# Kernel optimization log

Hardware: AMD Instinct MI355X
Metric: run time of the kernel (lower is better)

The kernel has to match this reference:

```python
import jax, jax.numpy as jnp
import numpy as np

B, L, D, P = 8, 2048, 1024, 4  # batch, length, word_dim, phrase_len


def setup_inputs() -> dict:
    key = jax.random.key(0)
    kx, kw, kb = jax.random.split(key, 3)
    x = jax.random.normal(kx, (B, L, D), dtype=jnp.float32)
    # torch nn.Linear(phrase_dim, word_dim): W [out=D, in=D*P], b [D]
    scale = 1.0 / np.sqrt(D * P)
    W = jax.random.uniform(kw, (D, D * P), dtype=jnp.float32, minval=-scale, maxval=scale)
    b = jax.random.uniform(kb, (D,), dtype=jnp.float32, minval=-scale, maxval=scale)
    return {"x": x, "W": W, "b": b}


def reference(x, W, b):
    Bs, Ls, Ds = x.shape
    Ps = W.shape[1] // Ds  # phrase_len
    # gram[i][:, t] = x[:, t - i] (zero for t < i): left-pad by i, keep first L steps.
    # Stack on the LAST axis then reshape, matching torch's contiguous view over
    # (dim, phrase_len) -> feature index d*P + i.
    grams = jnp.stack(
        [jnp.pad(x, ((0, 0), (i, 0), (0, 0)))[:, :Ls, :] for i in range(Ps)],
        axis=-1,
    )  # [B, L, D, P]
    feat = grams.reshape(Bs, Ls, Ds * Ps)  # [B, L, D*P]
    # nn.Linear: y = feat @ W.T + b
    return jnp.einsum("blf,df->bld", feat, W) + b
```

## Files before the change

### kernel.cpp

```cpp
#include <hip/hip_runtime.h>
#include <hip/hip_bf16.h>
#include <stdint.h>

#define Bq 8
#define Lq 2048
#define Dq 1024
#define Pq 4
#define Kq 4096
#define LPAD 2056
#define BM 256
#define BN 256
#define BK 64

typedef __attribute__((ext_vector_type(8))) short short8;
typedef __attribute__((ext_vector_type(4))) float f32x4;

__device__ __forceinline__ unsigned short f2bf(float f) {
  unsigned u = __float_as_uint(f);
  u += 0x7FFFu + ((u >> 16) & 1u);
  return (unsigned short)(u >> 16);
}

__device__ __forceinline__ void gload_lds16(const void* g, void* l) {
  __builtin_amdgcn_global_load_lds(
      (const __attribute__((address_space(1))) void*)g,
      (__attribute__((address_space(3))) void*)l, 16, 0, 0);
}

__global__ void k_prep(const float* __restrict__ x, const float* __restrict__ W,
                       unsigned short* __restrict__ xp, unsigned short* __restrict__ Wp) {
  if (blockIdx.x < 8224u) {
    unsigned g = blockIdx.x * blockDim.x + threadIdx.x;
    unsigned base = g * 8;
    const unsigned total = (unsigned)Bq * LPAD * Dq;
    if (base >= total) return;
    unsigned t = base >> 10;
    unsigned b = t / LPAD;
    unsigned r = t - b * LPAD;
    unsigned d = base & 1023;
    short8 o;
    if (r >= 3 && r < 3 + Lq) {
      const float* s = x + ((size_t)b * Lq + (r - 3)) * Dq + d;
      float4 v0 = *(const float4*)(s);
      float4 v1 = *(const float4*)(s + 4);
      o[0] = (short)f2bf(v0.x); o[1] = (short)f2bf(v0.y);
      o[2] = (short)f2bf(v0.z); o[3] = (short)f2bf(v0.w);
      o[4] = (short)f2bf(v1.x); o[5] = (short)f2bf(v1.y);
      o[6] = (short)f2bf(v1.z); o[7] = (short)f2bf(v1.w);
    } else {
      o = (short8)0;
    }
    *(short8*)(xp + base) = o;
  } else {
    unsigned g = (blockIdx.x - 8224u) * blockDim.x + threadIdx.x;
    unsigned base = g * 8;
    unsigned d = base >> 12;
    unsigned rem = base & 4095;
    unsigned dp = rem >> 2;
    const float4* src = (const float4*)(W + base);
    float4 v0 = src[0];
    float4 v1 = src[1];
    float a0[4] = {v0.x, v0.y, v0.z, v0.w};
    float a1[4] = {v1.x, v1.y, v1.z, v1.w};
#pragma unroll
    for (int i = 0; i < 4; ++i) {
      unsigned packed = (unsigned)f2bf(a0[i]) | ((unsigned)f2bf(a1[i]) << 16);
      *(unsigned*)(Wp + (size_t)d * 4096 + (size_t)i * 1024 + dp) = packed;
    }
  }
}


#define VM8 asm volatile("s_waitcnt vmcnt(8)" ::: "memory")
#define VM2 asm volatile("s_waitcnt vmcnt(2)" ::: "memory")
#define VM0 asm volatile("s_waitcnt vmcnt(0)" ::: "memory")
#define BAR __builtin_amdgcn_s_barrier()
#define NOPS ((void)0)

#define STAGE_A(buf, kt, h) do { \
    const unsigned scl_ = ((((unsigned)(bRow0 + (h) * 64 - ((kt) >> 4))) << 10) + (((unsigned)(kt) & 15u) << 6)) << 1; \
    _Pragma("unroll") for (int q_ = 0; q_ < 2; ++q_) \
      gload_lds16((const char*)xp + (thrA[q_] + scl_), \
                  lds + ((buf) << 15) + ((h) << 14) + (q_ << 13) + (tid << 4)); \
  } while (0)

#define STAGE_B(buf, kt, h) do { \
    const unsigned scl_ = ((((unsigned)(n0 + (h) * 32)) << 12) + ((unsigned)(kt) << 6)) << 1; \
    _Pragma("unroll") for (int q_ = 0; q_ < 2; ++q_) \
      gload_lds16((const char*)Wp + (thrB[q_] + scl_), \
                  lds + 65536 + ((buf) << 15) + ((h) << 14) + (q_ << 13) + (tid << 4)); \
  } while (0)

#define READ_A(dst, buf, h) do { \
    _Pragma("unroll") for (int mi = 0; mi < 4; ++mi) \
    _Pragma("unroll") for (int kk = 0; kk < 2; ++kk) \
      dst[mi][kk] = *(const short8*)(lds + (((buf) << 15) + ((h) << 14)) + aRC[mi][kk]); \
  } while (0)

#define READ_B(dst, buf, h) do { \
    _Pragma("unroll") for (int ni = 0; ni < 2; ++ni) \
    _Pragma("unroll") for (int kk = 0; kk < 2; ++kk) \
      dst[ni][kk] = *(const short8*)(lds + (((buf) << 15) + ((h) << 14)) + bRC[ni][kk]); \
  } while (0)

#define MFMA_PAIR(mh) do { \
    __builtin_amdgcn_s_setprio(1); \
    _Pragma("unroll") for (int kk = 0; kk < 2; ++kk) { \
      _Pragma("unroll") for (int mi = 0; mi < 4; ++mi) \
      _Pragma("unroll") for (int ni = 0; ni < 2; ++ni) \
        acc[(mh) * 4 + mi][ni] = __builtin_amdgcn_mfma_f32_16x16x32_bf16( \
            fa[mi][kk], bX[ni][kk], acc[(mh) * 4 + mi][ni], 0, 0, 0); \
      _Pragma("unroll") for (int mi = 0; mi < 4; ++mi) \
      _Pragma("unroll") for (int ni = 0; ni < 2; ++ni) \
        acc[(mh) * 4 + mi][2 + ni] = __builtin_amdgcn_mfma_f32_16x16x32_bf16( \
            fa[mi][kk], bY[ni][kk], acc[(mh) * 4 + mi][2 + ni], 0, 0, 0); \
    } \
    __builtin_amdgcn_s_setprio(0); \
  } while (0)

__global__ void __launch_bounds__(512, 2)
k_gemm(const unsigned short* __restrict__ xp,
       const unsigned short* __restrict__ Wp,
       const float* __restrict__ bias,
       float* __restrict__ out) {
  __shared__ __attribute__((aligned(16))) unsigned char lds[131072];

  const int tid  = threadIdx.x;
  const int lane = tid & 63;
  const int w    = tid >> 6;
  const int wm   = w >> 2;
  const int wn   = w & 3;

  const int bid = blockIdx.x;
  const int swz = (bid & 7) * 32 + (bid >> 3);
  const int m0 = (swz >> 2) * BM;
  const int n0 = (swz & 3) * BN;
  const int b  = m0 >> 11;
  const int l0 = m0 & 2047;
  const int bRow0 = b * LPAD + l0 + 3;

  const int sr0 = tid >> 3;
  const unsigned clog = ((unsigned)((tid & 7) ^ (sr0 & 7))) << 3;
  unsigned thrA[2], thrB[2];
  const unsigned nb0 = (((unsigned)sr0 >> 5) << 6) + ((unsigned)sr0 & 31);
#pragma unroll
  for (int q = 0; q < 2; ++q) {
    thrA[q] = ((((unsigned)(sr0 + q * 128)) << 10) + clog) << 1;
    thrB[q] = (((nb0 + q * 128u) << 12) + clog) << 1;
  }

  int aRC[4][2], bRC[2][2];
  {
    int colByte[2];
#pragma unroll
    for (int kk = 0; kk < 2; ++kk)
      colByte[kk] = (kk * 64 + ((lane >> 4) << 4)) ^ ((lane & 7) << 4);
#pragma unroll
    for (int mi = 0; mi < 4; ++mi)
#pragma unroll
      for (int kk = 0; kk < 2; ++kk)
        aRC[mi][kk] = ((wm * 64 + mi * 16 + (lane & 15)) << 7) + colByte[kk];
#pragma unroll
    for (int ni = 0; ni < 2; ++ni)
#pragma unroll
      for (int kk = 0; kk < 2; ++kk)
        bRC[ni][kk] = 65536 + ((wn * 32 + ni * 16 + (lane & 15)) << 7) + colByte[kk];
  }

  f32x4 acc[8][4] = {};
  short8 fa[4][2], bX[2][2], bY[2][2];

  STAGE_A(0, 0, 0);
  STAGE_B(0, 0, 0);
  STAGE_B(0, 0, 1);
  STAGE_A(0, 0, 1);
  STAGE_A(1, 1, 0);
  STAGE_B(1, 1, 0);
  STAGE_B(1, 1, 1);
  VM8;
  BAR;

#pragma unroll 1
  for (int it = 0; it < 31; ++it) {
    const int T = it * 2;
    READ_A(fa, 0, 0); READ_B(bX, 0, 0); READ_B(bY, 0, 1);
    STAGE_A(1, T + 1, 1);
    MFMA_PAIR(0);
    VM8;
    BAR;
    READ_A(fa, 0, 1);
    STAGE_A(0, T + 2, 0); STAGE_B(0, T + 2, 0); STAGE_B(0, T + 2, 1);
    MFMA_PAIR(1);
    VM8;
    BAR;
    READ_A(fa, 1, 0); READ_B(bX, 1, 0); READ_B(bY, 1, 1);
    STAGE_A(0, T + 2, 1);
    MFMA_PAIR(0);
    VM8;
    BAR;
    READ_A(fa, 1, 1);
    STAGE_A(1, T + 3, 0); STAGE_B(1, T + 3, 0); STAGE_B(1, T + 3, 1);
    MFMA_PAIR(1);
    VM8;
    BAR;
  }

  READ_A(fa, 0, 0); READ_B(bX, 0, 0); READ_B(bY, 0, 1);
  STAGE_A(1, 63, 1);
  MFMA_PAIR(0);
  VM8;
  BAR;
  READ_A(fa, 0, 1);
  MFMA_PAIR(1);
  VM2;
  BAR;
  READ_A(fa, 1, 0); READ_B(bX, 1, 0); READ_B(bY, 1, 1);
  MFMA_PAIR(0);
  VM0;
  BAR;
  READ_A(fa, 1, 1);
  MFMA_PAIR(1);

#pragma unroll
  for (int nig = 0; nig < 4; ++nig) {
    const int col = n0 + wn * 64 + nig * 16 + (lane & 15);
    const float bv = bias[col];
#pragma unroll
    for (int mig = 0; mig < 8; ++mig) {
      const int row0 = m0 + wm * 128 + mig * 16 + ((lane >> 4) << 2);
#pragma unroll
      for (int t2 = 0; t2 < 4; ++t2)
        out[(size_t)(row0 + t2) * Dq + col] = acc[mig][nig][t2] + bv;
    }
  }
}

__global__ void k_naive(const float* __restrict__ x, const float* __restrict__ W,
                        const float* __restrict__ bias, float* __restrict__ out) {
  size_t g = (size_t)blockIdx.x * blockDim.x + threadIdx.x;
  const size_t total = (size_t)Bq * Lq * Dq;
  if (g >= total) return;
  int d = (int)(g & 1023);
  int l = (int)((g >> 10) & 2047);
  int b = (int)(g >> 21);
  float s = bias[d];
  for (int i = 0; i < Pq; ++i) {
    if (l - i < 0) continue;
    const float* xr = x + ((size_t)b * Lq + (l - i)) * Dq;
    const float* wr = W + (size_t)d * Kq + i;
    float accv = 0.f;
    for (int dp = 0; dp < Dq; ++dp) accv += xr[dp] * wr[(size_t)dp * 4];
    s += accv;
  }
  out[g] = s;
}

extern "C" void kernel_launch(void* const* d_in, const int* in_sizes, int n_in,
                              void* d_out, int out_size, void* d_ws, size_t ws_size,
                              hipStream_t stream) {
  const float* x    = (const float*)d_in[0];
  const float* W    = (const float*)d_in[1];
  const float* bias = (const float*)d_in[2];
  float* out = (float*)d_out;

  const size_t WP_BYTES = (size_t)Dq * Kq * sizeof(unsigned short);
  const size_t XP_BYTES = (size_t)Bq * LPAD * Dq * sizeof(unsigned short);

  if (ws_size < WP_BYTES + XP_BYTES) {
    const size_t total = (size_t)Bq * Lq * Dq;
    k_naive<<<(unsigned)((total + 255) / 256), 256, 0, stream>>>(x, W, bias, out);
    return;
  }

  unsigned short* Wp = (unsigned short*)d_ws;
  unsigned short* xp = (unsigned short*)((char*)d_ws + WP_BYTES);

  k_prep<<<10272, 256, 0, stream>>>(x, W, xp, Wp);
  k_gemm<<<dim3((Bq * Lq / BM) * (Dq / BN)), 512, 0, stream>>>(xp, Wp, bias, out);
}
```

Before: 129.0 us.

## Double-buffer register fragments to overlap LDS reads with MFMA

Splits the A and B register fragments into two alternating sets, so the LDS reads for the next half-step are issued before the current MFMA batch runs instead of right after a barrier. The vmcnt waits are retuned to match the new staging order. Launch bounds drop to one block per SM so the extra fragment registers fit. The cost is a much larger register footprint and lower occupancy, which reduces latency hiding across blocks.

```diff
diff --git a/kernel.cpp b/kernel.cpp
--- a/kernel.cpp
+++ b/kernel.cpp
@@ -71,11 +71,10 @@
 }
 
 
-#define VM8 asm volatile("s_waitcnt vmcnt(8)" ::: "memory")
+#define VM6 asm volatile("s_waitcnt vmcnt(6)" ::: "memory")
 #define VM2 asm volatile("s_waitcnt vmcnt(2)" ::: "memory")
 #define VM0 asm volatile("s_waitcnt vmcnt(0)" ::: "memory")
 #define BAR __builtin_amdgcn_s_barrier()
-#define NOPS ((void)0)
 
 #define STAGE_A(buf, kt, h) do { \
     const unsigned scl_ = ((((unsigned)(bRow0 + (h) * 64 - ((kt) >> 4))) << 10) + (((unsigned)(kt) & 15u) << 6)) << 1; \
@@ -103,22 +102,22 @@
       dst[ni][kk] = *(const short8*)(lds + (((buf) << 15) + ((h) << 14)) + bRC[ni][kk]); \
   } while (0)
 
-#define MFMA_PAIR(mh) do { \
+#define MFMA_PAIR(mh, A, BX, BY) do { \
     __builtin_amdgcn_s_setprio(1); \
     _Pragma("unroll") for (int kk = 0; kk < 2; ++kk) { \
       _Pragma("unroll") for (int mi = 0; mi < 4; ++mi) \
       _Pragma("unroll") for (int ni = 0; ni < 2; ++ni) \
         acc[(mh) * 4 + mi][ni] = __builtin_amdgcn_mfma_f32_16x16x32_bf16( \
-            fa[mi][kk], bX[ni][kk], acc[(mh) * 4 + mi][ni], 0, 0, 0); \
+            A[mi][kk], BX[ni][kk], acc[(mh) * 4 + mi][ni], 0, 0, 0); \
       _Pragma("unroll") for (int mi = 0; mi < 4; ++mi) \
       _Pragma("unroll") for (int ni = 0; ni < 2; ++ni) \
         acc[(mh) * 4 + mi][2 + ni] = __builtin_amdgcn_mfma_f32_16x16x32_bf16( \
-            fa[mi][kk], bY[ni][kk], acc[(mh) * 4 + mi][2 + ni], 0, 0, 0); \
+            A[mi][kk], BY[ni][kk], acc[(mh) * 4 + mi][2 + ni], 0, 0, 0); \
     } \
     __builtin_amdgcn_s_setprio(0); \
   } while (0)
 
-__global__ void __launch_bounds__(512, 2)
+__global__ void __launch_bounds__(512, 1)
 k_gemm(const unsigned short* __restrict__ xp,
        const unsigned short* __restrict__ Wp,
        const float* __restrict__ bias,
@@ -168,7 +167,7 @@
   }
 
   f32x4 acc[8][4] = {};
-  short8 fa[4][2], bX[2][2], bY[2][2];
+  short8 a0[4][2], a1[4][2], bXe[2][2], bYe[2][2], bXo[2][2], bYo[2][2];
 
   STAGE_A(0, 0, 0);
   STAGE_B(0, 0, 0);
@@ -177,49 +176,41 @@
   STAGE_A(1, 1, 0);
   STAGE_B(1, 1, 0);
   STAGE_B(1, 1, 1);
-  VM8;
+  VM6;
   BAR;
+  READ_A(a0, 0, 0); READ_B(bXe, 0, 0); READ_B(bYe, 0, 1);
 
 #pragma unroll 1
   for (int it = 0; it < 31; ++it) {
     const int T = it * 2;
-    READ_A(fa, 0, 0); READ_B(bX, 0, 0); READ_B(bY, 0, 1);
+    READ_A(a1, 0, 1);
     STAGE_A(1, T + 1, 1);
-    MFMA_PAIR(0);
-    VM8;
-    BAR;
-    READ_A(fa, 0, 1);
+    MFMA_PAIR(0, a0, bXe, bYe);
+    VM2; BAR;
+    READ_A(a0, 1, 0); READ_B(bXo, 1, 0); READ_B(bYo, 1, 1);
     STAGE_A(0, T + 2, 0); STAGE_B(0, T + 2, 0); STAGE_B(0, T + 2, 1);
-    MFMA_PAIR(1);
-    VM8;
-    BAR;
-    READ_A(fa, 1, 0); READ_B(bX, 1, 0); READ_B(bY, 1, 1);
+    MFMA_PAIR(1, a1, bXe, bYe);
+    VM6; BAR;
+    READ_A(a1, 1, 1);
     STAGE_A(0, T + 2, 1);
-    MFMA_PAIR(0);
-    VM8;
-    BAR;
-    READ_A(fa, 1, 1);
+    MFMA_PAIR(0, a0, bXo, bYo);
+    VM2; BAR;
+    READ_A(a0, 0, 0); READ_B(bXe, 0, 0); READ_B(bYe, 0, 1);
     STAGE_A(1, T + 3, 0); STAGE_B(1, T + 3, 0); STAGE_B(1, T + 3, 1);
-    MFMA_PAIR(1);
-    VM8;
-    BAR;
-  }
-
-  READ_A(fa, 0, 0); READ_B(bX, 0, 0); READ_B(bY, 0, 1);
+    MFMA_PAIR(1, a1, bXo, bYo);
+    VM6; BAR;
+  }
+
+  READ_A(a1, 0, 1);
   STAGE_A(1, 63, 1);
-  MFMA_PAIR(0);
-  VM8;
-  BAR;
-  READ_A(fa, 0, 1);
-  MFMA_PAIR(1);
-  VM2;
-  BAR;
-  READ_A(fa, 1, 0); READ_B(bX, 1, 0); READ_B(bY, 1, 1);
-  MFMA_PAIR(0);
-  VM0;
-  BAR;
-  READ_A(fa, 1, 1);
-  MFMA_PAIR(1);
+  MFMA_PAIR(0, a0, bXe, bYe);
+  VM2; BAR;
+  READ_A(a0, 1, 0); READ_B(bXo, 1, 0); READ_B(bYo, 1, 1);
+  MFMA_PAIR(1, a1, bXe, bYe);
+  VM0; BAR;
+  READ_A(a1, 1, 1);
+  MFMA_PAIR(0, a0, bXo, bYo);
+  MFMA_PAIR(1, a1, bXo, bYo);
 
 #pragma unroll
   for (int nig = 0; nig < 4; ++nig) {
```

After: 358.1 us. 2.78x slower.
